# Optimization experiments

Hardware: AMD Instinct MI355X
Metric: run time of the kernel (lower is better)

Reference implementation:

```python
import jax, jax.numpy as jnp
import numpy as np

D_MODEL = 1024
HEAD = 16
D_K = D_MODEL // HEAD
NEG_INF = -1.0e9


def setup_inputs() -> dict:
    key = jax.random.key(0)
    ks = jax.random.split(key, 12)
    B, S = 2, 2048
    scale = 1.0 / np.sqrt(D_MODEL)
    inp = {
        "query": jax.random.normal(ks[0], (B, S, D_MODEL), jnp.float32),
        "key": jax.random.normal(ks[1], (B, S, D_MODEL), jnp.float32),
        "value": jax.random.normal(ks[2], (B, S, D_MODEL), jnp.float32),
        "mask": jax.random.randint(ks[3], (B, 1, 1, S), 0, 2, jnp.int32),
        "Wq": jax.random.normal(ks[4], (D_MODEL, D_MODEL), jnp.float32) * scale,
        "bq": jnp.zeros((D_MODEL,), jnp.float32),
        "Wk": jax.random.normal(ks[5], (D_MODEL, D_MODEL), jnp.float32) * scale,
        "bk": jnp.zeros((D_MODEL,), jnp.float32),
        "Wv": jax.random.normal(ks[6], (D_MODEL, D_MODEL), jnp.float32) * scale,
        "bv": jnp.zeros((D_MODEL,), jnp.float32),
        "Wo": jax.random.normal(ks[7], (D_MODEL, D_MODEL), jnp.float32) * scale,
        "bo": jnp.zeros((D_MODEL,), jnp.float32),
    }
    return inp


def reference(query, key, value, mask, Wq, bq, Wk, bk, Wv, bv, Wo, bo):
    B, S, _ = query.shape
    # QKV projections (torch nn.Linear: x @ W^T + b)
    q = query @ Wq.T + bq
    k = key @ Wk.T + bk
    v = value @ Wv.T + bv
    # [B, H, S, d_k]
    q = q.reshape(B, S, HEAD, D_K).transpose(0, 2, 1, 3)
    k = k.reshape(B, S, HEAD, D_K).transpose(0, 2, 1, 3)
    v = v.reshape(B, S, HEAD, D_K).transpose(0, 2, 1, 3)
    # scores [B, H, S, S]
    scores = jnp.einsum("bhqd,bhkd->bhqk", q, k) / jnp.sqrt(jnp.float32(D_K))
    scores = jnp.where(mask == 0, jnp.float32(NEG_INF), scores)
    attn = jax.nn.softmax(scores, axis=-1)  # dropout off (eval mode)
    ctx = jnp.einsum("bhqk,bhkd->bhqd", attn, v)
    ctx = ctx.transpose(0, 2, 1, 3).reshape(B, S, D_MODEL)
    return ctx @ Wo.T + bo
```

## Files before the change

kernel.cpp:

```cpp
#include <hip/hip_runtime.h>
#include <cstdint>
#include <cstddef>

typedef unsigned short u16;
typedef unsigned int   u32;
typedef __bf16 bf16x8 __attribute__((ext_vector_type(8)));
typedef float  f32x4  __attribute__((ext_vector_type(4)));

#define D_MODEL 1024
#define SEQ     2048
#define NTOK    4096
#define NHEAD   16
#define DK      64

#define FENCE() asm volatile("" ::: "memory")
#define SBAR()  asm volatile("s_barrier" ::: "memory")
#define WVL(N)  asm volatile("s_waitcnt vmcnt(" #N ") lgkmcnt(0)" ::: "memory")

__device__ __forceinline__ float fast_exp2(float x) {
  return __builtin_amdgcn_exp2f(x);
}

__device__ __forceinline__ u16 f2bf(float f) {
  u32 u = __builtin_bit_cast(u32, f);
  u += 0x7fffu + ((u >> 16) & 1u);
  return (u16)(u >> 16);
}

__device__ __forceinline__ u32 pkbf(float a, float b) {
  u16 x = __builtin_bit_cast(u16, (__bf16)a);
  u16 y = __builtin_bit_cast(u16, (__bf16)b);
  return (u32)x | ((u32)y << 16);
}

__device__ __forceinline__ void gload16(const u16* g, u16* l) {
  __builtin_amdgcn_global_load_lds(
      (__attribute__((address_space(1))) void*)(uintptr_t)g,
      (__attribute__((address_space(3))) void*)l,
      16, 0, 0);
}

__global__ __launch_bounds__(256) void scan_convert(
    const int* __restrict__ mask, int* __restrict__ idx, int* __restrict__ cnt,
    const float* __restrict__ wq, const float* __restrict__ wk,
    const float* __restrict__ wv, const float* __restrict__ wo,
    u16* __restrict__ wb) {
  __shared__ int sW[4];
  __shared__ int sTot;
  const int t = threadIdx.x;
  if (blockIdx.x < 2) {
    const int b = blockIdx.x;
    const int lane = t & 63, w = t >> 6;
    int m8[8];
    const int base = b * SEQ + t * 8;
    int tot = 0;
#pragma unroll
    for (int i = 0; i < 8; ++i) {
      m8[i] = (mask[base + i] != 0);
      tot += m8[i];
    }
    int v = tot;
#pragma unroll
    for (int d = 1; d < 64; d <<= 1) {
      int u = __shfl_up(v, d);
      if (lane >= d) v += u;
    }
    if (lane == 63) sW[w] = v;
    __syncthreads();
    if (t == 0) {
      int run = 0;
#pragma unroll
      for (int i = 0; i < 4; ++i) { int tmp = sW[i]; sW[i] = run; run += tmp; }
      sTot = run;
    }
    __syncthreads();
    int pos = v - tot + sW[w];
#pragma unroll
    for (int i = 0; i < 8; ++i)
      if (m8[i]) idx[b * SEQ + pos++] = t * 8 + i;
    const int cn = sTot;
    if (t == 0) cnt[b] = cn;
    for (int j = cn + t; j < SEQ; j += 256) idx[b * SEQ + j] = 0;
  } else {
    const int total = 1 << 20;
    for (int cid = (blockIdx.x - 2) * 256 + t; cid < total; cid += 1024 * 256) {
      int which = cid >> 18;
      int off = cid & ((1 << 18) - 1);
      const float* src =
          which == 0 ? wq : (which == 1 ? wk : (which == 2 ? wv : wo));
      u16* dst = wb + ((size_t)which << 20);
      float4 f = ((const float4*)src)[off];
      ushort4 u;
      u.x = f2bf(f.x); u.y = f2bf(f.y); u.z = f2bf(f.z); u.w = f2bf(f.w);
      ((ushort4*)dst)[off] = u;
    }
  }
}

__global__ __launch_bounds__(256, 3) void gemm_qkv(
    const float* __restrict__ Aq, const float* __restrict__ Ak,
    const float* __restrict__ Av, const u16* __restrict__ Bw,
    const float* __restrict__ b0, const float* __restrict__ b1,
    const float* __restrict__ b2, u16* __restrict__ Cout) {
  __shared__ __align__(16) u16 smem[3 * 128 * 64];
  u16* sA = smem;

  const int t = threadIdx.x;
  const int z = blockIdx.z;
  const float* Ap = (z == 0) ? Aq : ((z == 1) ? Ak : Av);
  const u16* Bp = Bw + ((size_t)z << 20);
  const float* bias = (z == 0) ? b0 : ((z == 1) ? b1 : b2);
  const float scl = (z == 0) ? 0.18033688011f : 1.0f;

  const int m0 = blockIdx.x * 128, n0 = blockIdx.y * 128;
  const int lane = t & 63, wv = t >> 6;
  const int wm = (wv >> 1) * 64, wn = (wv & 1) * 64;
  const int c = lane & 15, qd = lane >> 4;

  const int arow = t >> 3;
  const int aoff = (((t & 7) - arow) & 7) * 8;
  const float* gaA = Ap + (size_t)(m0 + arow) * D_MODEL + aoff;
  const u16* gaB = Bp + (size_t)(n0 + arow) * D_MODEL + aoff;

  float4 pa[4][2];
  u32 cv[4][4];

#pragma unroll
  for (int j = 0; j < 4; ++j) {
    pa[j][0] = *(const float4*)(gaA + (size_t)(32 * j) * D_MODEL);
    pa[j][1] = *(const float4*)(gaA + (size_t)(32 * j) * D_MODEL + 4);
  }
  FENCE();
#pragma unroll
  for (int j = 0; j < 4; ++j)
    gload16(gaB + (size_t)(32 * j) * D_MODEL, smem + 8192 + (t + 256 * j) * 8);
  WVL(4);
#pragma unroll
  for (int j = 0; j < 4; ++j) {
    cv[j][0] = pkbf(pa[j][0].x, pa[j][0].y);
    cv[j][1] = pkbf(pa[j][0].z, pa[j][0].w);
    cv[j][2] = pkbf(pa[j][1].x, pa[j][1].y);
    cv[j][3] = pkbf(pa[j][1].z, pa[j][1].w);
  }
  FENCE();
#pragma unroll
  for (int j = 0; j < 4; ++j) {
    pa[j][0] = *(const float4*)(gaA + 64 + (size_t)(32 * j) * D_MODEL);
    pa[j][1] = *(const float4*)(gaA + 64 + (size_t)(32 * j) * D_MODEL + 4);
  }
  FENCE();
#pragma unroll
  for (int j = 0; j < 4; ++j) {
    uint4 v4 = {cv[j][0], cv[j][1], cv[j][2], cv[j][3]};
    *(uint4*)&sA[(t + 256 * j) * 8] = v4;
  }

  f32x4 acc[4][4] = {};

#pragma unroll
  for (int kbi = 0; kbi < 16; ++kbi) {
    const int cur = kbi & 1;
    if (kbi == 15) { WVL(0); } else { WVL(8); }
    SBAR();
    if (kbi + 1 < 16) {
      u16* sBn = smem + 8192 + (1 - cur) * 8192;
      const int kb2 = (kbi + 1) * 64;
#pragma unroll
      for (int j = 0; j < 4; ++j)
        gload16(gaB + kb2 + (size_t)(32 * j) * D_MODEL, sBn + (t + 256 * j) * 8);
    }
    FENCE();
    const u16* sB = smem + 8192 + cur * 8192;
#pragma unroll
    for (int s = 0; s < 2; ++s) {
      const int ao = ((s * 4 + qd + wm + c) & 7) * 8;
      const int bo = ((s * 4 + qd + wn + c) & 7) * 8;
      bf16x8 af[4], bfr[4];
#pragma unroll
      for (int i = 0; i < 4; ++i)
        af[i] = *(const bf16x8*)&sA[(wm + i * 16 + c) * 64 + ao];
#pragma unroll
      for (int j = 0; j < 4; ++j)
        bfr[j] = *(const bf16x8*)&sB[(wn + j * 16 + c) * 64 + bo];
#pragma unroll
      for (int i = 0; i < 4; ++i)
#pragma unroll
        for (int j = 0; j < 4; ++j)
          acc[i][j] = __builtin_amdgcn_mfma_f32_16x16x32_bf16(af[i], bfr[j],
                                                              acc[i][j], 0, 0, 0);
    }
    if (kbi + 1 < 16) {
      WVL(4);
#pragma unroll
      for (int j = 0; j < 4; ++j) {
        cv[j][0] = pkbf(pa[j][0].x, pa[j][0].y);
        cv[j][1] = pkbf(pa[j][0].z, pa[j][0].w);
        cv[j][2] = pkbf(pa[j][1].x, pa[j][1].y);
        cv[j][3] = pkbf(pa[j][1].z, pa[j][1].w);
      }
      if (kbi + 2 < 16) {
        const int kb3 = (kbi + 2) * 64;
#pragma unroll
        for (int j = 0; j < 4; ++j) {
          pa[j][0] = *(const float4*)(gaA + kb3 + (size_t)(32 * j) * D_MODEL);
          pa[j][1] = *(const float4*)(gaA + kb3 + (size_t)(32 * j) * D_MODEL + 4);
        }
      }
      FENCE();
      SBAR();
#pragma unroll
      for (int j = 0; j < 4; ++j) {
        uint4 v4 = {cv[j][0], cv[j][1], cv[j][2], cv[j][3]};
        *(uint4*)&sA[(t + 256 * j) * 8] = v4;
      }
    }
  }
  __syncthreads();

  u16* sC = smem;
  if (z == 2) {
#pragma unroll
    for (int j = 0; j < 4; ++j) {
      const int col = wn + j * 16 + c;
      const float bv = bias[n0 + col];
#pragma unroll
      for (int i = 0; i < 4; ++i)
#pragma unroll
        for (int r = 0; r < 4; ++r)
          sC[col * 136 + wm + i * 16 + qd * 4 + r] = f2bf(acc[i][j][r] + bv);
    }
    __syncthreads();
    u16* VT = Cout + ((size_t)2 << 22);
    const int bb = m0 >> 11, s0 = m0 & 2047;
    const int sidx = (t & 15) * 8;
#pragma unroll
    for (int outer = 0; outer < 8; ++outer) {
      const int vrow = outer * 16 + (t >> 4);
      const int col = n0 + vrow;
      const int hh = col >> 6, dd = col & 63;
      uint4 val = *(const uint4*)&sC[vrow * 136 + sidx];
      *(uint4*)&VT[((size_t)((bb * NHEAD + hh) * DK + dd)) * SEQ + s0 + sidx] =
          val;
    }
  } else {
#pragma unroll
    for (int j = 0; j < 4; ++j) {
      const int col = wn + j * 16 + c;
      const float bv = bias[n0 + col];
#pragma unroll
      for (int i = 0; i < 4; ++i)
#pragma unroll
        for (int r = 0; r < 4; ++r)
          sC[(wm + i * 16 + qd * 4 + r) * 136 + col] =
              f2bf((acc[i][j][r] + bv) * scl);
    }
    __syncthreads();
    u16* outp = Cout + ((size_t)z << 22);
    const int cidx = (t & 15) * 8;
#pragma unroll
    for (int outer = 0; outer < 8; ++outer) {
      const int lrow = outer * 16 + (t >> 4);
      uint4 val = *(const uint4*)&sC[lrow * 136 + cidx];
      *(uint4*)&outp[(size_t)(m0 + lrow) * D_MODEL + n0 + cidx] = val;
    }
  }
}

__global__ __launch_bounds__(256) void vtc_gather(const u16* __restrict__ VT,
                                                  const int* __restrict__ idx,
                                                  const int* __restrict__ cnt,
                                                  u16* __restrict__ VTc) {
  const int row = blockIdx.x;
  const int b = row >> 10;
  const int cn = cnt[b];
  const u16* src = VT + (size_t)row * SEQ;
  u16* dst = VTc + (size_t)row * SEQ;
  const int* ib = idx + b * SEQ;
  for (int j = threadIdx.x; j < cn; j += 256) dst[j] = src[ib[j]];
}

__global__ __launch_bounds__(256) void mha_attn(
    const u16* __restrict__ QKVb, const u16* __restrict__ VTc,
    const int* __restrict__ idx, const int* __restrict__ cnt,
    u16* __restrict__ Opart, float* __restrict__ ml) {
  __shared__ __align__(16) u16 sK[64 * 72];
  __shared__ __align__(16) u16 sVt[64 * 72];
  __shared__ __align__(16) u16 sP[128 * 72];

  const int t = threadIdx.x, lane = t & 63, wq = t >> 6;
  const int c = lane & 15, qd = lane >> 4;
  const int qb = blockIdx.x, h = blockIdx.y;
  const int b = blockIdx.z & 1, ck = blockIdx.z >> 1;

  const int cn = cnt[b];
  const int nb = (cn + 63) >> 6;
  const int half = (nb + 1) >> 1;
  const int kstart = ck ? half : 0;
  const int kend = ck ? nb : half;

  const u16* Qg = QKVb;
  const u16* Kg = QKVb + ((size_t)4 << 20);
  const u16* VTch = VTc + ((size_t)((b * NHEAD + h) * DK)) * SEQ;
  const int rowbase = b * SEQ;
  const int colbase = h * DK;

  bf16x8 aq[2][2];
#pragma unroll
  for (int qt = 0; qt < 2; ++qt) {
    const u16* g = Qg +
                   (size_t)(rowbase + qb * 128 + wq * 32 + qt * 16 + c) * D_MODEL +
                   colbase + qd * 8;
    aq[qt][0] = *(const bf16x8*)g;
    aq[qt][1] = *(const bf16x8*)(g + 32);
  }

  float l[2] = {0.f, 0.f};
  f32x4 o[2][4] = {};
  const float MADD = -1.4426950e9f;
  const float MFIX = 16.0f;

  const int r0s = t >> 2, offs = (t & 3) * 16;
  const u16* gvb = VTch + (size_t)r0s * SEQ + offs;
  const int* idxb = idx + b * SEQ + r0s;

  uint4 k0, k1, v0, v1;
  int sNext2 = 0;
  if (kstart < kend) {
    const int s0i = idxb[kstart * 64];
    const u16* gk = Kg + (size_t)(rowbase + s0i) * D_MODEL + colbase + offs;
    const u16* gv = gvb + kstart * 64;
    k0 = *(const uint4*)gk;
    k1 = *(const uint4*)(gk + 8);
    v0 = *(const uint4*)gv;
    v1 = *(const uint4*)(gv + 8);
    if (kstart + 1 < kend) sNext2 = idxb[(kstart + 1) * 64];
  }

  for (int kbi = kstart; kbi < kend; ++kbi) {
    __syncthreads();
    *(uint4*)&sK[r0s * 72 + offs] = k0;
    *(uint4*)&sK[r0s * 72 + offs + 8] = k1;
    *(uint4*)&sVt[r0s * 72 + offs] = v0;
    *(uint4*)&sVt[r0s * 72 + offs + 8] = v1;
    __syncthreads();
    if (kbi + 1 < kend) {
      const u16* gk = Kg + (size_t)(rowbase + sNext2) * D_MODEL + colbase + offs;
      const u16* gv = gvb + (kbi + 1) * 64;
      k0 = *(const uint4*)gk;
      k1 = *(const uint4*)(gk + 8);
      v0 = *(const uint4*)gv;
      v1 = *(const uint4*)(gv + 8);
    }
    if (kbi + 2 < kend) sNext2 = idxb[(kbi + 2) * 64];

    const bool full = ((kbi + 1) << 6) <= cn;
    f32x4 st[2][4];
#pragma unroll
    for (int tt = 0; tt < 4; ++tt) {
      bf16x8 ak0 = *(const bf16x8*)&sK[(tt * 16 + c) * 72 + qd * 8];
      bf16x8 ak1 = *(const bf16x8*)&sK[(tt * 16 + c) * 72 + qd * 8 + 32];
      f32x4 cin;
      if (full) {
        cin = f32x4{0.f, 0.f, 0.f, 0.f};
      } else {
        const int jb = (kbi << 6) + tt * 16 + qd * 4;
        cin = f32x4{jb + 0 < cn ? 0.f : MADD, jb + 1 < cn ? 0.f : MADD,
                    jb + 2 < cn ? 0.f : MADD, jb + 3 < cn ? 0.f : MADD};
      }
#pragma unroll
      for (int qt = 0; qt < 2; ++qt) {
        f32x4 a =
            __builtin_amdgcn_mfma_f32_16x16x32_bf16(ak0, aq[qt][0], cin, 0, 0, 0);
        a = __builtin_amdgcn_mfma_f32_16x16x32_bf16(ak1, aq[qt][1], a, 0, 0, 0);
        st[qt][tt] = a;
      }
    }

#pragma unroll
    for (int qt = 0; qt < 2; ++qt) {
      float sum = 0.f;
      const int prow = (wq * 32 + qt * 16 + c) * 72;
#pragma unroll
      for (int tt = 0; tt < 4; ++tt) {
        u32 pk[2];
#pragma unroll
        for (int pr = 0; pr < 2; ++pr) {
          u32 p0 = __builtin_bit_cast(u32, fast_exp2(st[qt][tt][2 * pr] - MFIX));
          u32 p1 =
              __builtin_bit_cast(u32, fast_exp2(st[qt][tt][2 * pr + 1] - MFIX));
          u32 hi1 = p1 & 0xffff0000u;
          pk[pr] = (p0 >> 16) | hi1;
          sum += __builtin_bit_cast(float, p0 & 0xffff0000u);
          sum += __builtin_bit_cast(float, hi1);
        }
        uint2 pv2 = {pk[0], pk[1]};
        *(uint2*)&sP[prow + tt * 16 + qd * 4] = pv2;
      }
      l[qt] += sum;
    }

    bf16x8 bp[2][2];
#pragma unroll
    for (int qt = 0; qt < 2; ++qt) {
      const int prow = (wq * 32 + qt * 16 + c) * 72;
      bp[qt][0] = *(const bf16x8*)&sP[prow + qd * 8];
      bp[qt][1] = *(const bf16x8*)&sP[prow + qd * 8 + 32];
    }
#pragma unroll
    for (int dt = 0; dt < 4; ++dt) {
      bf16x8 av0 = *(const bf16x8*)&sVt[(dt * 16 + c) * 72 + qd * 8];
      bf16x8 av1 = *(const bf16x8*)&sVt[(dt * 16 + c) * 72 + qd * 8 + 32];
#pragma unroll
      for (int qt = 0; qt < 2; ++qt) {
        o[qt][dt] =
            __builtin_amdgcn_mfma_f32_16x16x32_bf16(av0, bp[qt][0], o[qt][dt], 0, 0, 0);
        o[qt][dt] =
            __builtin_amdgcn_mfma_f32_16x16x32_bf16(av1, bp[qt][1], o[qt][dt], 0, 0, 0);
      }
    }
  }

  const size_t obase =
      (size_t)ck * 4194304 + ((size_t)((b * NHEAD + h) * SEQ) + qb * 128) * 64;
  const int mlbase = ((ck * 2 + b) * NHEAD + h) * SEQ + qb * 128;
#pragma unroll
  for (int qt = 0; qt < 2; ++qt) {
    float ls = l[qt];
    ls += __shfl_xor(ls, 16);
    ls += __shfl_xor(ls, 32);
    const float inv = (ls != 0.f) ? 1.0f / ls : 0.f;
    const int q = wq * 32 + qt * 16 + c;
#pragma unroll
    for (int dt = 0; dt < 4; ++dt) {
      u32 lo = (u32)f2bf(o[qt][dt][0] * inv) |
               ((u32)f2bf(o[qt][dt][1] * inv) << 16);
      u32 hi = (u32)f2bf(o[qt][dt][2] * inv) |
               ((u32)f2bf(o[qt][dt][3] * inv) << 16);
      uint2 ov = {lo, hi};
      *(uint2*)&Opart[obase + (size_t)q * 64 + dt * 16 + qd * 4] = ov;
    }
    if (qd == 0) ml[mlbase + q] = ls;
  }
}

__global__ __launch_bounds__(256) void mha_combine(
    const u16* __restrict__ Opart, const float* __restrict__ ml,
    u16* __restrict__ ctx) {
  const int tid = blockIdx.x * 256 + threadIdx.x;
  const int row = tid >> 3, d0 = (tid & 7) * 8;
  const int b = row >> 15, h = (row >> 11) & 15, q = row & 2047;
  float l1 = ml[row];
  float l2 = ml[65536 + row];
  float inv = 1.0f / (l1 + l2);
  float w1 = l1 * inv, w2 = l2 * inv;
  const size_t o1 = (size_t)row * 64 + d0;
  uint4 pa = *(const uint4*)(Opart + o1);
  uint4 pb = *(const uint4*)(Opart + 4194304 + o1);
  u32 wa[4] = {pa.x, pa.y, pa.z, pa.w};
  u32 wb[4] = {pb.x, pb.y, pb.z, pb.w};
  u32 out[4];
#pragma unroll
  for (int j = 0; j < 4; ++j) {
    float alo = __builtin_bit_cast(float, wa[j] << 16);
    float ahi = __builtin_bit_cast(float, wa[j] & 0xffff0000u);
    float blo = __builtin_bit_cast(float, wb[j] << 16);
    float bhi = __builtin_bit_cast(float, wb[j] & 0xffff0000u);
    float rlo = w1 * alo + w2 * blo;
    float rhi = w1 * ahi + w2 * bhi;
    out[j] = (u32)f2bf(rlo) | ((u32)f2bf(rhi) << 16);
  }
  uint4 ov = {out[0], out[1], out[2], out[3]};
  *(uint4*)&ctx[((size_t)(b * SEQ + q)) * D_MODEL + h * DK + d0] = ov;
}

__global__ __launch_bounds__(256) void gemm_out(
    const u16* __restrict__ A, const u16* __restrict__ Bw,
    const float* __restrict__ bias, float* __restrict__ Cout) {
  __shared__ __align__(16) u16 sAb[3][128 * 64];
  __shared__ __align__(16) u16 sBc[3][64 * 64];

  const int t = threadIdx.x;
  const int m0 = blockIdx.x * 128, n0 = blockIdx.y * 64;
  const int lane = t & 63, wv = t >> 6;
  const int wm = (wv >> 1) * 64, wn = (wv & 1) * 32;
  const int c = lane & 15, qd = lane >> 4;

  const int arow = t >> 3;
  const int aoff = (((t & 7) - arow) & 7) * 8;
  const u16* gaA = A + (size_t)(m0 + arow) * D_MODEL + aoff;
  const u16* gaB = Bw + (size_t)(n0 + arow) * D_MODEL + aoff;

#pragma unroll
  for (int j = 0; j < 4; ++j)
    gload16(gaA + (size_t)(32 * j) * D_MODEL, &sAb[0][(t + 256 * j) * 8]);
#pragma unroll
  for (int j = 0; j < 2; ++j)
    gload16(gaB + (size_t)(32 * j) * D_MODEL, &sBc[0][(t + 256 * j) * 8]);
  FENCE();
#pragma unroll
  for (int j = 0; j < 4; ++j)
    gload16(gaA + 64 + (size_t)(32 * j) * D_MODEL, &sAb[1][(t + 256 * j) * 8]);
#pragma unroll
  for (int j = 0; j < 2; ++j)
    gload16(gaB + 64 + (size_t)(32 * j) * D_MODEL, &sBc[1][(t + 256 * j) * 8]);
  FENCE();

  f32x4 acc[4][2] = {};

  for (int kbi = 0; kbi < 16; ++kbi) {
    const int cur = kbi % 3;
    if (kbi == 15) { WVL(0); } else { WVL(6); }
    SBAR();
    if (kbi + 2 < 16) {
      const int nxt = (kbi + 2) % 3;
      const int kb2 = (kbi + 2) * 64;
#pragma unroll
      for (int j = 0; j < 4; ++j)
        gload16(gaA + kb2 + (size_t)(32 * j) * D_MODEL,
                &sAb[nxt][(t + 256 * j) * 8]);
#pragma unroll
      for (int j = 0; j < 2; ++j)
        gload16(gaB + kb2 + (size_t)(32 * j) * D_MODEL,
                &sBc[nxt][(t + 256 * j) * 8]);
      FENCE();
    }
    const u16* sA = sAb[cur];
    const u16* sB = sBc[cur];
#pragma unroll
    for (int s = 0; s < 2; ++s) {
      const int ao = ((s * 4 + qd + wm + c) & 7) * 8;
      const int bo = ((s * 4 + qd + wn + c) & 7) * 8;
      bf16x8 af[4], bfr[2];
#pragma unroll
      for (int i = 0; i < 4; ++i)
        af[i] = *(const bf16x8*)&sA[(wm + i * 16 + c) * 64 + ao];
#pragma unroll
      for (int j = 0; j < 2; ++j)
        bfr[j] = *(const bf16x8*)&sB[(wn + j * 16 + c) * 64 + bo];
#pragma unroll
      for (int i = 0; i < 4; ++i)
#pragma unroll
        for (int j = 0; j < 2; ++j)
          acc[i][j] = __builtin_amdgcn_mfma_f32_16x16x32_bf16(af[i], bfr[j],
                                                              acc[i][j], 0, 0, 0);
    }
  }

#pragma unroll
  for (int j = 0; j < 2; ++j) {
    const int col = n0 + wn + j * 16 + c;
    const float bv = bias[col];
#pragma unroll
    for (int i = 0; i < 4; ++i)
#pragma unroll
      for (int r = 0; r < 4; ++r) {
        const int row = m0 + wm + i * 16 + qd * 4 + r;
        Cout[(size_t)row * D_MODEL + col] = acc[i][j][r] + bv;
      }
  }
}

extern "C" void kernel_launch(void* const* d_in, const int* in_sizes, int n_in,
                              void* d_out, int out_size, void* d_ws,
                              size_t ws_size, hipStream_t stream) {
  const float* query = (const float*)d_in[0];
  const float* key   = (const float*)d_in[1];
  const float* value = (const float*)d_in[2];
  const int*   mask  = (const int*)d_in[3];
  const float* Wq = (const float*)d_in[4];
  const float* bq = (const float*)d_in[5];
  const float* Wk = (const float*)d_in[6];
  const float* bk = (const float*)d_in[7];
  const float* Wv = (const float*)d_in[8];
  const float* bv = (const float*)d_in[9];
  const float* Wo = (const float*)d_in[10];
  const float* bo = (const float*)d_in[11];

  u16* ws  = (u16*)d_ws;
  u16* Wb  = ws + ((size_t)12 << 20);
  u16* QKV = ws + ((size_t)16 << 20);
  u16* CTX = ws + ((size_t)28 << 20);
  u16* VTc = ws;
  u16* Opart = ws + ((size_t)4 << 20);
  float* ml = (float*)(ws + ((size_t)12 << 20));
  int* idxp = (int*)(ws + ((size_t)28 << 20));
  int* cntp = idxp + 2 * SEQ;

  scan_convert<<<dim3(1026), dim3(256), 0, stream>>>(mask, idxp, cntp, Wq, Wk,
                                                     Wv, Wo, Wb);
  gemm_qkv<<<dim3(32, 8, 3), dim3(256), 0, stream>>>(query, key, value, Wb, bq,
                                                     bk, bv, QKV);
  vtc_gather<<<dim3(2048), dim3(256), 0, stream>>>(QKV + ((size_t)8 << 20), idxp,
                                                   cntp, VTc);
  mha_attn<<<dim3(16, 16, 4), dim3(256), 0, stream>>>(QKV, VTc, idxp, cntp,
                                                      Opart, ml);
  mha_combine<<<dim3(2048), dim3(256), 0, stream>>>(Opart, ml, CTX);
  gemm_out<<<dim3(32, 16), dim3(256), 0, stream>>>(CTX, Wb + ((size_t)3 << 20),
                                                   bo, (float*)d_out);
}
```

Baseline: 206.5 us.

## Fuse split-KV combine into output projection GEMM A-tile loading

Removes the separate mha_combine kernel: the output GEMM now loads both partial attention outputs and their softmax denominators directly, merges them in registers, and writes the combined bf16 tile to shared memory as its A operand. The ml buffer layout is interleaved per row so both partial sums load as one float2. This saves a kernel launch and the write and reread of the CTX buffer. In exchange, each of the 16 output-column blocks recomputes the combine for its rows, so partial outputs are read many times. The A tile also moves from async copies to a register path, and occupancy is hinted at 2 blocks.

```diff
diff --git a/kernel.cpp b/kernel.cpp
--- a/kernel.cpp
+++ b/kernel.cpp
@@ -422,7 +422,7 @@
 
   const size_t obase =
       (size_t)ck * 4194304 + ((size_t)((b * NHEAD + h) * SEQ) + qb * 128) * 64;
-  const int mlbase = ((ck * 2 + b) * NHEAD + h) * SEQ + qb * 128;
+  const int mlb2 = (((b * NHEAD + h) * SEQ) + qb * 128) * 2 + ck;
 #pragma unroll
   for (int qt = 0; qt < 2; ++qt) {
     float ls = l[qt];
@@ -439,45 +439,16 @@
       uint2 ov = {lo, hi};
       *(uint2*)&Opart[obase + (size_t)q * 64 + dt * 16 + qd * 4] = ov;
     }
-    if (qd == 0) ml[mlbase + q] = ls;
-  }
-}
-
-__global__ __launch_bounds__(256) void mha_combine(
-    const u16* __restrict__ Opart, const float* __restrict__ ml,
-    u16* __restrict__ ctx) {
-  const int tid = blockIdx.x * 256 + threadIdx.x;
-  const int row = tid >> 3, d0 = (tid & 7) * 8;
-  const int b = row >> 15, h = (row >> 11) & 15, q = row & 2047;
-  float l1 = ml[row];
-  float l2 = ml[65536 + row];
-  float inv = 1.0f / (l1 + l2);
-  float w1 = l1 * inv, w2 = l2 * inv;
-  const size_t o1 = (size_t)row * 64 + d0;
-  uint4 pa = *(const uint4*)(Opart + o1);
-  uint4 pb = *(const uint4*)(Opart + 4194304 + o1);
-  u32 wa[4] = {pa.x, pa.y, pa.z, pa.w};
-  u32 wb[4] = {pb.x, pb.y, pb.z, pb.w};
-  u32 out[4];
-#pragma unroll
-  for (int j = 0; j < 4; ++j) {
-    float alo = __builtin_bit_cast(float, wa[j] << 16);
-    float ahi = __builtin_bit_cast(float, wa[j] & 0xffff0000u);
-    float blo = __builtin_bit_cast(float, wb[j] << 16);
-    float bhi = __builtin_bit_cast(float, wb[j] & 0xffff0000u);
-    float rlo = w1 * alo + w2 * blo;
-    float rhi = w1 * ahi + w2 * bhi;
-    out[j] = (u32)f2bf(rlo) | ((u32)f2bf(rhi) << 16);
-  }
-  uint4 ov = {out[0], out[1], out[2], out[3]};
-  *(uint4*)&ctx[((size_t)(b * SEQ + q)) * D_MODEL + h * DK + d0] = ov;
-}
-
-__global__ __launch_bounds__(256) void gemm_out(
-    const u16* __restrict__ A, const u16* __restrict__ Bw,
-    const float* __restrict__ bias, float* __restrict__ Cout) {
-  __shared__ __align__(16) u16 sAb[3][128 * 64];
-  __shared__ __align__(16) u16 sBc[3][64 * 64];
+    if (qd == 0) ml[mlb2 + q * 2] = ls;
+  }
+}
+
+__global__ __launch_bounds__(256, 2) void gemm_out(
+    const u16* __restrict__ Opart, const float* __restrict__ ml2,
+    const u16* __restrict__ Bw, const float* __restrict__ bias,
+    float* __restrict__ Cout) {
+  __shared__ __align__(16) u16 smem[16384];
+  u16* sA = smem;
 
   const int t = threadIdx.x;
   const int m0 = blockIdx.x * 128, n0 = blockIdx.y * 64;
@@ -487,45 +458,73 @@
 
   const int arow = t >> 3;
   const int aoff = (((t & 7) - arow) & 7) * 8;
-  const u16* gaA = A + (size_t)(m0 + arow) * D_MODEL + aoff;
+  const int token = m0 + arow;
+  const int bb = token >> 11, q0r = token & 2047;
+  const u16* gaA1 = Opart + ((size_t)(bb * 16) * 2048 + q0r) * 64 + aoff;
+  const u16* gaA2 = gaA1 + ((size_t)4 << 20);
+  const float* gml = ml2 + ((size_t)(bb * 16) * 2048 + q0r) * 2;
   const u16* gaB = Bw + (size_t)(n0 + arow) * D_MODEL + aoff;
 
-#pragma unroll
-  for (int j = 0; j < 4; ++j)
-    gload16(gaA + (size_t)(32 * j) * D_MODEL, &sAb[0][(t + 256 * j) * 8]);
+  uint4 pa1[4], pa2[4];
+  float2 mlv[4];
+  u32 cv[4][4];
+
+#define COMBINE_STEP()                                                        \
+  _Pragma("unroll") for (int j = 0; j < 4; ++j) {                             \
+    float l1 = mlv[j].x, l2 = mlv[j].y;                                       \
+    float inv = 1.0f / (l1 + l2);                                             \
+    float w1 = l1 * inv, w2 = l2 * inv;                                       \
+    u32 wa[4] = {pa1[j].x, pa1[j].y, pa1[j].z, pa1[j].w};                     \
+    u32 wb_[4] = {pa2[j].x, pa2[j].y, pa2[j].z, pa2[j].w};                    \
+    _Pragma("unroll") for (int w = 0; w < 4; ++w) {                           \
+      float alo = __builtin_bit_cast(float, wa[w] << 16);                     \
+      float ahi = __builtin_bit_cast(float, wa[w] & 0xffff0000u);             \
+      float blo = __builtin_bit_cast(float, wb_[w] << 16);                    \
+      float bhi = __builtin_bit_cast(float, wb_[w] & 0xffff0000u);            \
+      cv[j][w] = pkbf(w1 * alo + w2 * blo, w1 * ahi + w2 * bhi);              \
+    }                                                                         \
+  }
+
+#define ISSUE_AGROUP(KK)                                                      \
+  _Pragma("unroll") for (int j = 0; j < 4; ++j)                               \
+      pa1[j] = *(const uint4*)(gaA1 + (size_t)(KK)*131072 + 2048 * j);        \
+  _Pragma("unroll") for (int j = 0; j < 4; ++j)                               \
+      pa2[j] = *(const uint4*)(gaA2 + (size_t)(KK)*131072 + 2048 * j);        \
+  _Pragma("unroll") for (int j = 0; j < 4; ++j)                               \
+      mlv[j] = *(const float2*)(gml + (size_t)(KK)*4096 + 64 * j);
+
+  ISSUE_AGROUP(0);
+  FENCE();
 #pragma unroll
   for (int j = 0; j < 2; ++j)
-    gload16(gaB + (size_t)(32 * j) * D_MODEL, &sBc[0][(t + 256 * j) * 8]);
+    gload16(gaB + (size_t)(32 * j) * D_MODEL, smem + 8192 + (t + 256 * j) * 8);
+  WVL(2);
+  COMBINE_STEP();
   FENCE();
-#pragma unroll
-  for (int j = 0; j < 4; ++j)
-    gload16(gaA + 64 + (size_t)(32 * j) * D_MODEL, &sAb[1][(t + 256 * j) * 8]);
-#pragma unroll
-  for (int j = 0; j < 2; ++j)
-    gload16(gaB + 64 + (size_t)(32 * j) * D_MODEL, &sBc[1][(t + 256 * j) * 8]);
+  ISSUE_AGROUP(1);
   FENCE();
+#pragma unroll
+  for (int j = 0; j < 4; ++j) {
+    uint4 v4 = {cv[j][0], cv[j][1], cv[j][2], cv[j][3]};
+    *(uint4*)&sA[(t + 256 * j) * 8] = v4;
+  }
 
   f32x4 acc[4][2] = {};
 
+#pragma unroll
   for (int kbi = 0; kbi < 16; ++kbi) {
-    const int cur = kbi % 3;
-    if (kbi == 15) { WVL(0); } else { WVL(6); }
+    const int cur = kbi & 1;
+    if (kbi == 15) { WVL(0); } else { WVL(12); }
     SBAR();
-    if (kbi + 2 < 16) {
-      const int nxt = (kbi + 2) % 3;
-      const int kb2 = (kbi + 2) * 64;
-#pragma unroll
-      for (int j = 0; j < 4; ++j)
-        gload16(gaA + kb2 + (size_t)(32 * j) * D_MODEL,
-                &sAb[nxt][(t + 256 * j) * 8]);
+    if (kbi + 1 < 16) {
+      u16* sBn = smem + 8192 + (1 - cur) * 4096;
+      const int kb2 = (kbi + 1) * 64;
 #pragma unroll
       for (int j = 0; j < 2; ++j)
-        gload16(gaB + kb2 + (size_t)(32 * j) * D_MODEL,
-                &sBc[nxt][(t + 256 * j) * 8]);
-      FENCE();
-    }
-    const u16* sA = sAb[cur];
-    const u16* sB = sBc[cur];
+        gload16(gaB + kb2 + (size_t)(32 * j) * D_MODEL, sBn + (t + 256 * j) * 8);
+    }
+    FENCE();
+    const u16* sB = smem + 8192 + cur * 4096;
 #pragma unroll
     for (int s = 0; s < 2; ++s) {
       const int ao = ((s * 4 + qd + wm + c) & 7) * 8;
@@ -544,7 +543,21 @@
           acc[i][j] = __builtin_amdgcn_mfma_f32_16x16x32_bf16(af[i], bfr[j],
                                                               acc[i][j], 0, 0, 0);
     }
-  }
+    if (kbi + 1 < 16) {
+      WVL(2);
+      COMBINE_STEP();
+      if (kbi + 2 < 16) { ISSUE_AGROUP(kbi + 2); }
+      FENCE();
+      SBAR();
+#pragma unroll
+      for (int j = 0; j < 4; ++j) {
+        uint4 v4 = {cv[j][0], cv[j][1], cv[j][2], cv[j][3]};
+        *(uint4*)&sA[(t + 256 * j) * 8] = v4;
+      }
+    }
+  }
+#undef COMBINE_STEP
+#undef ISSUE_AGROUP
 
 #pragma unroll
   for (int j = 0; j < 2; ++j) {
@@ -579,7 +592,6 @@
   u16* ws  = (u16*)d_ws;
   u16* Wb  = ws + ((size_t)12 << 20);
   u16* QKV = ws + ((size_t)16 << 20);
-  u16* CTX = ws + ((size_t)28 << 20);
   u16* VTc = ws;
   u16* Opart = ws + ((size_t)4 << 20);
   float* ml = (float*)(ws + ((size_t)12 << 20));
@@ -594,7 +606,7 @@
                                                    cntp, VTc);
   mha_attn<<<dim3(16, 16, 4), dim3(256), 0, stream>>>(QKV, VTc, idxp, cntp,
                                                       Opart, ml);
-  mha_combine<<<dim3(2048), dim3(256), 0, stream>>>(Opart, ml, CTX);
-  gemm_out<<<dim3(32, 16), dim3(256), 0, stream>>>(CTX, Wb + ((size_t)3 << 20),
-                                                   bo, (float*)d_out);
-}
+  gemm_out<<<dim3(32, 16), dim3(256), 0, stream>>>(Opart, ml,
+                                                   Wb + ((size_t)3 << 20), bo,
+                                                   (float*)d_out);
+}
```

Measured after the change: 221.2 us. 1.07x slower.
